# Performance work log

Hardware: AMD Instinct MI355X
Metric: run time of the kernel (lower is better)

## Reference

```python
import jax, jax.numpy as jnp
import numpy as np

N = 2048
D_IN = 128
D_OUT = 128
H = 8
EDGE_DIM = 8
EDGE_HID = 32
NEG_SLOPE = 0.2


def setup_inputs() -> dict:
    key = jax.random.key(0)
    ks = jax.random.split(key, 9)
    return {
        "inputs": jax.random.normal(ks[0], (N, D_IN), dtype=jnp.float32),
        "adj": jax.random.randint(ks[1], (N, N), 0, 2, dtype=jnp.int32),
        "edge_attr": jax.random.normal(ks[2], (N, N, EDGE_DIM), dtype=jnp.float32),
        # Linear weights stored as [in, out] (y = x @ W)
        "Wq": jax.random.normal(ks[3], (D_IN, D_OUT), dtype=jnp.float32) * 0.05,
        "Wk": jax.random.normal(ks[4], (D_IN, D_OUT), dtype=jnp.float32) * 0.05,
        "Wv": jax.random.normal(ks[5], (D_IN, D_OUT), dtype=jnp.float32) * 0.05,
        "We": jax.random.normal(ks[6], (EDGE_DIM, EDGE_HID), dtype=jnp.float32) * 0.05,
        "Wr": jax.random.normal(ks[7], (EDGE_HID, D_OUT), dtype=jnp.float32) * 0.05,
        "Wo": jax.random.normal(ks[8], (D_OUT, D_OUT), dtype=jnp.float32) * 0.05,
    }


def reference(inputs, adj, edge_attr, Wq, Wk, Wv, We, Wr, Wo):
    n = inputs.shape[0]
    dh = D_OUT // H  # head dim = 16
    # Projections -> [H, N, dh]
    Q = (inputs @ Wq).reshape(n, H, dh).transpose(1, 0, 2)
    K = (inputs @ Wk).reshape(n, H, dh).transpose(1, 0, 2)
    V = (inputs @ Wv).reshape(n, H, dh).transpose(1, 0, 2)
    # Edge bias: r_ij = W_r(W_e(e_ij)) viewed per-head; bias_hij = q_hi . r_ijh.
    # Fold We@Wr and contract with Q first to avoid materializing [N,N,D_OUT].
    Wer = (We @ Wr).reshape(EDGE_DIM, H, dh)          # [E, H, dh]
    QW = jnp.einsum('hid,ehd->hie', Q, Wer)           # [H, N, E]
    scores = (jnp.einsum('hid,hjd->hij', Q, K)
              + jnp.einsum('hie,ije->hij', QW, edge_attr)) / jnp.sqrt(jnp.float32(dh))
    scores = jax.nn.leaky_relu(scores, NEG_SLOPE)
    # Adjacency mask: only attend along existing edges
    scores = jnp.where((adj > 0)[None, :, :], scores, jnp.float32(-1e9))
    attn = jax.nn.softmax(scores, axis=-1)            # dropout is identity in eval
    out = jnp.einsum('hij,hjd->hid', attn, V)         # [H, N, dh]
    out = out.transpose(1, 0, 2).reshape(n, D_OUT)
    return out @ Wo
```

## Files before the change

kernel.cpp:

```cpp
#include <hip/hip_runtime.h>
#include <math.h>

#define NN 2048
#define DD 128
#define HH 8
#define DHH 16
#define EDIM 8
#define EHID 32

__global__ __launch_bounds__(384) void proj_kernel(
    const float* __restrict__ X,
    const float* __restrict__ Wq, const float* __restrict__ Wk,
    const float* __restrict__ Wv, const float* __restrict__ We,
    const float* __restrict__ Wr,
    float* __restrict__ Qo, float* __restrict__ Ko,
    float* __restrict__ Vo, float* __restrict__ QWo) {
  __shared__ float x_lds[2][128];
  __shared__ float wer_lds[8][128];
  __shared__ float q_lds[2][128];
  const int t = threadIdx.x;
  const int i0 = blockIdx.x * 2;

  if (t < 256) x_lds[t >> 7][t & 127] = X[(size_t)i0 * 128 + t];

  if (t < 128) {
    float acc[EDIM];
#pragma unroll
    for (int e = 0; e < EDIM; ++e) acc[e] = 0.f;
    for (int k = 0; k < EHID; ++k) {
      const float wr = Wr[k * 128 + t];
#pragma unroll
      for (int e = 0; e < EDIM; ++e) acc[e] = fmaf(We[e * EHID + k], wr, acc[e]);
    }
#pragma unroll
    for (int e = 0; e < EDIM; ++e) wer_lds[e][t] = acc[e];
  }
  __syncthreads();

  const int mat = t >> 7;
  const int c = t & 127;
  const float* __restrict__ W = (mat == 0) ? Wq : ((mat == 1) ? Wk : Wv);
  float a0 = 0.f, a1 = 0.f;
#pragma unroll 8
  for (int d = 0; d < 128; ++d) {
    const float w = W[d * 128 + c];
    a0 = fmaf(x_lds[0][d], w, a0);
    a1 = fmaf(x_lds[1][d], w, a1);
  }
  float* __restrict__ Out = (mat == 0) ? Qo : ((mat == 1) ? Ko : Vo);
  Out[(size_t)i0 * 128 + c] = a0;
  Out[(size_t)(i0 + 1) * 128 + c] = a1;
  if (mat == 0) { q_lds[0][c] = a0; q_lds[1][c] = a1; }
  __syncthreads();

  if (t < 64) {
    const int h = t >> 3, e = t & 7;
#pragma unroll
    for (int r = 0; r < 2; ++r) {
      float s = 0.f;
#pragma unroll
      for (int d = 0; d < DHH; ++d)
        s = fmaf(q_lds[r][h * DHH + d], wer_lds[e][h * DHH + d], s);
      QWo[(size_t)(i0 + r) * 64 + h * 8 + e] = s;
    }
  }
}

#define LOADEK(S, P) do {                                           \
    const int _j0 = (P) * 2;                                        \
    const float4* _e = ep + 2 * _j0;                                \
    e##S##0 = _e[0]; e##S##1 = _e[1]; e##S##2 = _e[2]; e##S##3 = _e[3]; \
    const float4* _k = kp + (size_t)_j0 * 32;                       \
    k##S##0 = _k[0];  k##S##1 = _k[1];  k##S##2 = _k[2];  k##S##3 = _k[3]; \
    k##S##4 = _k[32]; k##S##5 = _k[33]; k##S##6 = _k[34]; k##S##7 = _k[35]; \
  } while (0)

__global__ __launch_bounds__(512) void attn_kernel(
    const float* __restrict__ Qg, const float* __restrict__ Kg,
    const float* __restrict__ Vg, const float* __restrict__ QWg,
    const int* __restrict__ adj, const float* __restrict__ Eg,
    const float* __restrict__ Wo, float* __restrict__ out) {
  const int t = threadIdx.x;
  const int il = t & 3;
  const int h = (t >> 2) & 7;
  const int jo = t >> 5;
  const int i0 = blockIdx.x * 4;
  const int i = i0 + il;

  float4 q0, q1, q2, q3, qw0, qw1;
  {
    const float4* qp = (const float4*)(Qg + (size_t)i * 128 + h * 16);
    q0 = qp[0]; q1 = qp[1]; q2 = qp[2]; q3 = qp[3];
    const float4* wp = (const float4*)(QWg + (size_t)i * 64 + h * 8);
    qw0 = wp[0]; qw1 = wp[1];
  }

  float acc[16];
#pragma unroll
  for (int d = 0; d < 16; ++d) acc[d] = 0.f;
  float m = -INFINITY, mt = -INFINITY, l = 0.f;

  const int jbase = jo * 128;
  const int4* __restrict__ ap4 = (const int4*)(adj + (size_t)i * NN + jbase);
  const float4* __restrict__ ep = (const float4*)Eg + ((size_t)i * NN + jbase) * 2;
  const float4* __restrict__ kp = (const float4*)Kg + (size_t)jbase * 32 + h * 4;
  const float4* __restrict__ vp = (const float4*)Vg + (size_t)jbase * 32 + h * 4;

  auto score = [&](const float4 E0, const float4 E1,
                   const float4 K0, const float4 K1, const float4 K2, const float4 K3,
                   const int a) -> float {
    float s0 = q0.x * K0.x;    s0 = fmaf(q0.y, K0.y, s0);
    s0 = fmaf(q0.z, K0.z, s0); s0 = fmaf(q0.w, K0.w, s0);
    s0 = fmaf(q1.x, K1.x, s0); s0 = fmaf(q1.y, K1.y, s0);
    s0 = fmaf(q1.z, K1.z, s0); s0 = fmaf(q1.w, K1.w, s0);
    float s1 = q2.x * K2.x;    s1 = fmaf(q2.y, K2.y, s1);
    s1 = fmaf(q2.z, K2.z, s1); s1 = fmaf(q2.w, K2.w, s1);
    s1 = fmaf(q3.x, K3.x, s1); s1 = fmaf(q3.y, K3.y, s1);
    s1 = fmaf(q3.z, K3.z, s1); s1 = fmaf(q3.w, K3.w, s1);
    float b0 = qw0.x * E0.x;   b0 = fmaf(qw0.y, E0.y, b0);
    b0 = fmaf(qw0.z, E0.z, b0); b0 = fmaf(qw0.w, E0.w, b0);
    b0 = fmaf(qw1.x, E1.x, b0); b0 = fmaf(qw1.y, E1.y, b0);
    b0 = fmaf(qw1.z, E1.z, b0); b0 = fmaf(qw1.w, E1.w, b0);
    const float raw = (s0 + s1) + b0;
    float sc2 = fmaf(0.14426950f, fabsf(raw), 0.21640425f * raw);
    sc2 = (a > 0) ? sc2 : -1e9f;
    if (sc2 > mt) {
      const float r = exp2f(m - sc2);
      l *= r;
#pragma unroll
      for (int d = 0; d < 16; ++d) acc[d] *= r;
      m = sc2; mt = sc2 + 12.f;
    }
    const float p = exp2f(sc2 - m);
    l += p;
    return p;
  };
  auto pv = [&](const float p, const float4 V0, const float4 V1,
                const float4 V2, const float4 V3) {
    acc[0]  = fmaf(p, V0.x, acc[0]);  acc[1]  = fmaf(p, V0.y, acc[1]);
    acc[2]  = fmaf(p, V0.z, acc[2]);  acc[3]  = fmaf(p, V0.w, acc[3]);
    acc[4]  = fmaf(p, V1.x, acc[4]);  acc[5]  = fmaf(p, V1.y, acc[5]);
    acc[6]  = fmaf(p, V1.z, acc[6]);  acc[7]  = fmaf(p, V1.w, acc[7]);
    acc[8]  = fmaf(p, V2.x, acc[8]);  acc[9]  = fmaf(p, V2.y, acc[9]);
    acc[10] = fmaf(p, V2.z, acc[10]); acc[11] = fmaf(p, V2.w, acc[11]);
    acc[12] = fmaf(p, V3.x, acc[12]); acc[13] = fmaf(p, V3.y, acc[13]);
    acc[14] = fmaf(p, V3.z, acc[14]); acc[15] = fmaf(p, V3.w, acc[15]);
  };

  float4 eA0, eA1, eA2, eA3, kA0, kA1, kA2, kA3, kA4, kA5, kA6, kA7;
  float4 eB0, eB1, eB2, eB3, kB0, kB1, kB2, kB3, kB4, kB5, kB6, kB7;

  int4 a_cur = ap4[0];
  LOADEK(A, 0);
#pragma unroll 1
  for (int p2 = 0; p2 < 64; p2 += 2) {
    const int g = p2 >> 1;
    const int4 a_nxt = ap4[g < 31 ? g + 1 : 31];
    LOADEK(B, p2 + 1);
    {
      const float4* _v = vp + (size_t)(p2 * 2) * 32;
      const float4 v0 = _v[0],  v1 = _v[1],  v2 = _v[2],  v3 = _v[3];
      const float4 v4 = _v[32], v5 = _v[33], v6 = _v[34], v7 = _v[35];
      const float pa = score(eA0, eA1, kA0, kA1, kA2, kA3, a_cur.x);
      pv(pa, v0, v1, v2, v3);
      const float pb = score(eA2, eA3, kA4, kA5, kA6, kA7, a_cur.y);
      pv(pb, v4, v5, v6, v7);
    }
    LOADEK(A, p2 + 2 < 64 ? p2 + 2 : 63);
    {
      const float4* _v = vp + (size_t)(p2 * 2 + 2) * 32;
      const float4 v0 = _v[0],  v1 = _v[1],  v2 = _v[2],  v3 = _v[3];
      const float4 v4 = _v[32], v5 = _v[33], v6 = _v[34], v7 = _v[35];
      const float pa = score(eB0, eB1, kB0, kB1, kB2, kB3, a_cur.z);
      pv(pa, v0, v1, v2, v3);
      const float pb = score(eB2, eB3, kB4, kB5, kB6, kB7, a_cur.w);
      pv(pb, v4, v5, v6, v7);
    }
    a_cur = a_nxt;
  }

  __shared__ float mbuf[256 * 18];
  __shared__ float o_lds[4][128];
  const int u = t & 31;
  for (int k = 8; k >= 1; k >>= 1) {
    if (jo >= k && jo < 2 * k) {
      float* b = mbuf + ((size_t)((jo - k) * 32 + u)) * 18;
      b[0] = m; b[1] = l;
#pragma unroll
      for (int d = 0; d < 16; ++d) b[2 + d] = acc[d];
    }
    __syncthreads();
    if (jo < k) {
      const float* b = mbuf + ((size_t)(jo * 32 + u)) * 18;
      const float m2 = b[0], l2 = b[1];
      const float M = fmaxf(m, m2);
      const float sa = exp2f(m - M);
      const float sb = exp2f(m2 - M);
      l = l * sa + l2 * sb;
#pragma unroll
      for (int d = 0; d < 16; ++d) acc[d] = acc[d] * sa + b[2 + d] * sb;
      m = M;
    }
    __syncthreads();
  }

  if (jo == 0) {
    const float inv = 1.f / l;
#pragma unroll
    for (int d = 0; d < 16; ++d) o_lds[il][h * 16 + d] = acc[d] * inv;
  }
  __syncthreads();

  const int r = t >> 7;
  const int c = t & 127;
  float s = 0.f;
#pragma unroll 8
  for (int d = 0; d < 128; ++d)
    s = fmaf(o_lds[r][d], Wo[d * 128 + c], s);
  out[(size_t)(i0 + r) * 128 + c] = s;
}

extern "C" void kernel_launch(void* const* d_in, const int* in_sizes, int n_in,
                              void* d_out, int out_size, void* d_ws, size_t ws_size,
                              hipStream_t stream) {
  const float* X   = (const float*)d_in[0];
  const int*   adj = (const int*)d_in[1];
  const float* E   = (const float*)d_in[2];
  const float* Wq  = (const float*)d_in[3];
  const float* Wk  = (const float*)d_in[4];
  const float* Wv  = (const float*)d_in[5];
  const float* We  = (const float*)d_in[6];
  const float* Wr  = (const float*)d_in[7];
  const float* Wo  = (const float*)d_in[8];
  float* out = (float*)d_out;

  float* Qs  = (float*)d_ws;
  float* Ks  = Qs + (size_t)NN * DD;
  float* Vs  = Ks + (size_t)NN * DD;
  float* QWs = Vs + (size_t)NN * DD;

  hipLaunchKernelGGL(proj_kernel, dim3(NN / 2), dim3(384), 0, stream,
                     X, Wq, Wk, Wv, We, Wr, Qs, Ks, Vs, QWs);
  hipLaunchKernelGGL(attn_kernel, dim3(NN / 4), dim3(512), 0, stream,
                     Qs, Ks, Vs, QWs, adj, E, Wo, out);
}
```

Before: 442.3 us.

## Warp-specialize attention with async global-to-LDS producer and ring buffer

The attention kernel is split into a producer wave and consumer waves. The producer wave streams K, V and edge-attribute tiles into a 4-slot LDS ring with global_load_lds and vmcnt waits. The consumer waves read these tiles from LDS and run the online-softmax accumulation, with the two roles kept in step by matched s_barrier calls. Blocks now cover 2 query rows instead of 4. The aim is to overlap global loads with compute and share K/V through LDS instead of per-thread global loads. In exchange the kernel adds a barrier per key step, gets less K/V reuse per block, and relies on the barrier counts of both roles matching exactly.

```diff
diff --git a/kernel.cpp b/kernel.cpp
--- a/kernel.cpp
+++ b/kernel.cpp
@@ -7,6 +7,9 @@
 #define DHH 16
 #define EDIM 8
 #define EHID 32
+
+typedef __attribute__((address_space(1))) const void GV;
+typedef __attribute__((address_space(3))) void LV;
 
 __global__ __launch_bounds__(384) void proj_kernel(
     const float* __restrict__ X,
@@ -66,158 +69,194 @@
   }
 }
 
-#define LOADEK(S, P) do {                                           \
-    const int _j0 = (P) * 2;                                        \
-    const float4* _e = ep + 2 * _j0;                                \
-    e##S##0 = _e[0]; e##S##1 = _e[1]; e##S##2 = _e[2]; e##S##3 = _e[3]; \
-    const float4* _k = kp + (size_t)_j0 * 32;                       \
-    k##S##0 = _k[0];  k##S##1 = _k[1];  k##S##2 = _k[2];  k##S##3 = _k[3]; \
-    k##S##4 = _k[32]; k##S##5 = _k[33]; k##S##6 = _k[34]; k##S##7 = _k[35]; \
-  } while (0)
-
-__global__ __launch_bounds__(512) void attn_kernel(
+__global__ __launch_bounds__(320) void attn_kernel(
     const float* __restrict__ Qg, const float* __restrict__ Kg,
     const float* __restrict__ Vg, const float* __restrict__ QWg,
     const int* __restrict__ adj, const float* __restrict__ Eg,
     const float* __restrict__ Wo, float* __restrict__ out) {
+  __shared__ float4 Ks_lds[4][512];
+  __shared__ float4 Vs_lds[4][512];
+  __shared__ float4 Es_lds[4][64];
+  __shared__ float mbuf[128 * 18];
+  __shared__ float o_lds[2][128];
+
   const int t = threadIdx.x;
-  const int il = t & 3;
-  const int h = (t >> 2) & 7;
-  const int jo = t >> 5;
-  const int i0 = blockIdx.x * 4;
-  const int i = i0 + il;
-
-  float4 q0, q1, q2, q3, qw0, qw1;
-  {
-    const float4* qp = (const float4*)(Qg + (size_t)i * 128 + h * 16);
-    q0 = qp[0]; q1 = qp[1]; q2 = qp[2]; q3 = qp[3];
-    const float4* wp = (const float4*)(QWg + (size_t)i * 64 + h * 8);
-    qw0 = wp[0]; qw1 = wp[1];
-  }
-
-  float acc[16];
-#pragma unroll
-  for (int d = 0; d < 16; ++d) acc[d] = 0.f;
-  float m = -INFINITY, mt = -INFINITY, l = 0.f;
-
-  const int jbase = jo * 128;
-  const int4* __restrict__ ap4 = (const int4*)(adj + (size_t)i * NN + jbase);
-  const float4* __restrict__ ep = (const float4*)Eg + ((size_t)i * NN + jbase) * 2;
-  const float4* __restrict__ kp = (const float4*)Kg + (size_t)jbase * 32 + h * 4;
-  const float4* __restrict__ vp = (const float4*)Vg + (size_t)jbase * 32 + h * 4;
-
-  auto score = [&](const float4 E0, const float4 E1,
-                   const float4 K0, const float4 K1, const float4 K2, const float4 K3,
-                   const int a) -> float {
-    float s0 = q0.x * K0.x;    s0 = fmaf(q0.y, K0.y, s0);
-    s0 = fmaf(q0.z, K0.z, s0); s0 = fmaf(q0.w, K0.w, s0);
-    s0 = fmaf(q1.x, K1.x, s0); s0 = fmaf(q1.y, K1.y, s0);
-    s0 = fmaf(q1.z, K1.z, s0); s0 = fmaf(q1.w, K1.w, s0);
-    float s1 = q2.x * K2.x;    s1 = fmaf(q2.y, K2.y, s1);
-    s1 = fmaf(q2.z, K2.z, s1); s1 = fmaf(q2.w, K2.w, s1);
-    s1 = fmaf(q3.x, K3.x, s1); s1 = fmaf(q3.y, K3.y, s1);
-    s1 = fmaf(q3.z, K3.z, s1); s1 = fmaf(q3.w, K3.w, s1);
-    float b0 = qw0.x * E0.x;   b0 = fmaf(qw0.y, E0.y, b0);
-    b0 = fmaf(qw0.z, E0.z, b0); b0 = fmaf(qw0.w, E0.w, b0);
-    b0 = fmaf(qw1.x, E1.x, b0); b0 = fmaf(qw1.y, E1.y, b0);
-    b0 = fmaf(qw1.z, E1.z, b0); b0 = fmaf(qw1.w, E1.w, b0);
-    const float raw = (s0 + s1) + b0;
-    float sc2 = fmaf(0.14426950f, fabsf(raw), 0.21640425f * raw);
-    sc2 = (a > 0) ? sc2 : -1e9f;
-    if (sc2 > mt) {
-      const float r = exp2f(m - sc2);
-      l *= r;
-#pragma unroll
-      for (int d = 0; d < 16; ++d) acc[d] *= r;
-      m = sc2; mt = sc2 + 12.f;
-    }
-    const float p = exp2f(sc2 - m);
-    l += p;
-    return p;
-  };
-  auto pv = [&](const float p, const float4 V0, const float4 V1,
-                const float4 V2, const float4 V3) {
-    acc[0]  = fmaf(p, V0.x, acc[0]);  acc[1]  = fmaf(p, V0.y, acc[1]);
-    acc[2]  = fmaf(p, V0.z, acc[2]);  acc[3]  = fmaf(p, V0.w, acc[3]);
-    acc[4]  = fmaf(p, V1.x, acc[4]);  acc[5]  = fmaf(p, V1.y, acc[5]);
-    acc[6]  = fmaf(p, V1.z, acc[6]);  acc[7]  = fmaf(p, V1.w, acc[7]);
-    acc[8]  = fmaf(p, V2.x, acc[8]);  acc[9]  = fmaf(p, V2.y, acc[9]);
-    acc[10] = fmaf(p, V2.z, acc[10]); acc[11] = fmaf(p, V2.w, acc[11]);
-    acc[12] = fmaf(p, V3.x, acc[12]); acc[13] = fmaf(p, V3.y, acc[13]);
-    acc[14] = fmaf(p, V3.z, acc[14]); acc[15] = fmaf(p, V3.w, acc[15]);
-  };
-
-  float4 eA0, eA1, eA2, eA3, kA0, kA1, kA2, kA3, kA4, kA5, kA6, kA7;
-  float4 eB0, eB1, eB2, eB3, kB0, kB1, kB2, kB3, kB4, kB5, kB6, kB7;
-
-  int4 a_cur = ap4[0];
-  LOADEK(A, 0);
-#pragma unroll 1
-  for (int p2 = 0; p2 < 64; p2 += 2) {
-    const int g = p2 >> 1;
-    const int4 a_nxt = ap4[g < 31 ? g + 1 : 31];
-    LOADEK(B, p2 + 1);
+  const int i0 = blockIdx.x * 2;
+
+  if (t >= 256) {
+    const int lid = t - 256;
+    const int hi = lid >> 5;
+    const int r = lid & 31;
+    const int h_p = r & 7, qq_p = r >> 3;
+    const float* Kbase = Kg + (size_t)hi * 16384 + h_p * 16 + qq_p * 4;
+    const float* Vbase = Vg + (size_t)hi * 16384 + h_p * 16 + qq_p * 4;
+    const int il_e = lid >> 5;
+    const int jo_e = (lid & 31) >> 1, half = lid & 1;
+    const float* Ebase = Eg + ((size_t)(i0 + il_e) * 2048 + jo_e * 128) * 8 + half * 4;
+
+    auto ISSUE = [&](int slot, int jj) {
+      const float* kb = Kbase + (size_t)jj * 128;
+      const float* vb = Vbase + (size_t)jj * 128;
+      const float* eb = Ebase + (size_t)jj * 8;
+#pragma unroll
+      for (int j = 0; j < 8; ++j)
+        __builtin_amdgcn_global_load_lds((GV*)(kb + j * 32768),
+                                         (LV*)&Ks_lds[slot][j * 64], 16, 0, 0);
+#pragma unroll
+      for (int j = 0; j < 8; ++j)
+        __builtin_amdgcn_global_load_lds((GV*)(vb + j * 32768),
+                                         (LV*)&Vs_lds[slot][j * 64], 16, 0, 0);
+      __builtin_amdgcn_global_load_lds((GV*)eb, (LV*)&Es_lds[slot][0], 16, 0, 0);
+    };
+
+    ISSUE(0, 0); ISSUE(1, 1); ISSUE(2, 2);
+    asm volatile("s_waitcnt vmcnt(34)" ::: "memory");
+    __builtin_amdgcn_s_barrier();
+    __builtin_amdgcn_sched_barrier(0);
+    for (int jj = 0; jj < 128; ++jj) {
+      if (jj < 125) {
+        ISSUE((jj + 3) & 3, jj + 3);
+        asm volatile("s_waitcnt vmcnt(34)" ::: "memory");
+      } else if (jj == 125) {
+        asm volatile("s_waitcnt vmcnt(17)" ::: "memory");
+      } else {
+        asm volatile("s_waitcnt vmcnt(0)" ::: "memory");
+      }
+      __builtin_amdgcn_s_barrier();
+      __builtin_amdgcn_sched_barrier(0);
+    }
+  } else {
+    const int il = t & 1;
+    const int h = (t >> 1) & 7;
+    const int jo = t >> 4;
+    const int i = i0 + il;
+
+    float4 q0, q1, q2, q3, qw0, qw1;
     {
-      const float4* _v = vp + (size_t)(p2 * 2) * 32;
-      const float4 v0 = _v[0],  v1 = _v[1],  v2 = _v[2],  v3 = _v[3];
-      const float4 v4 = _v[32], v5 = _v[33], v6 = _v[34], v7 = _v[35];
-      const float pa = score(eA0, eA1, kA0, kA1, kA2, kA3, a_cur.x);
-      pv(pa, v0, v1, v2, v3);
-      const float pb = score(eA2, eA3, kA4, kA5, kA6, kA7, a_cur.y);
-      pv(pb, v4, v5, v6, v7);
-    }
-    LOADEK(A, p2 + 2 < 64 ? p2 + 2 : 63);
+      const float4* qp = (const float4*)(Qg + (size_t)i * 128 + h * 16);
+      q0 = qp[0]; q1 = qp[1]; q2 = qp[2]; q3 = qp[3];
+      const float4* wp = (const float4*)(QWg + (size_t)i * 64 + h * 8);
+      qw0 = wp[0]; qw1 = wp[1];
+    }
+
+    float acc[16];
+#pragma unroll
+    for (int d = 0; d < 16; ++d) acc[d] = 0.f;
+    float m = -INFINITY, mt = -INFINITY, l = 0.f;
+
+    const int4* __restrict__ ap4 = (const int4*)(adj + (size_t)i * NN + jo * 128);
+
+    auto score = [&](const float4 E0, const float4 E1,
+                     const float4 K0, const float4 K1, const float4 K2,
+                     const float4 K3, const int a) -> float {
+      float s0 = q0.x * K0.x;    s0 = fmaf(q0.y, K0.y, s0);
+      s0 = fmaf(q0.z, K0.z, s0); s0 = fmaf(q0.w, K0.w, s0);
+      s0 = fmaf(q1.x, K1.x, s0); s0 = fmaf(q1.y, K1.y, s0);
+      s0 = fmaf(q1.z, K1.z, s0); s0 = fmaf(q1.w, K1.w, s0);
+      float s1 = q2.x * K2.x;    s1 = fmaf(q2.y, K2.y, s1);
+      s1 = fmaf(q2.z, K2.z, s1); s1 = fmaf(q2.w, K2.w, s1);
+      s1 = fmaf(q3.x, K3.x, s1); s1 = fmaf(q3.y, K3.y, s1);
+      s1 = fmaf(q3.z, K3.z, s1); s1 = fmaf(q3.w, K3.w, s1);
+      float b0 = qw0.x * E0.x;    b0 = fmaf(qw0.y, E0.y, b0);
+      b0 = fmaf(qw0.z, E0.z, b0); b0 = fmaf(qw0.w, E0.w, b0);
+      b0 = fmaf(qw1.x, E1.x, b0); b0 = fmaf(qw1.y, E1.y, b0);
+      b0 = fmaf(qw1.z, E1.z, b0); b0 = fmaf(qw1.w, E1.w, b0);
+      const float raw = (s0 + s1) + b0;
+      float sc2 = fmaf(0.14426950f, fabsf(raw), 0.21640425f * raw);
+      sc2 = (a > 0) ? sc2 : -1e9f;
+      if (sc2 > mt) {
+        const float rr = exp2f(m - sc2);
+        l *= rr;
+#pragma unroll
+        for (int d = 0; d < 16; ++d) acc[d] *= rr;
+        m = sc2; mt = sc2 + 12.f;
+      }
+      const float p = exp2f(sc2 - m);
+      l += p;
+      return p;
+    };
+    auto pv = [&](const float p, const float4 V0, const float4 V1,
+                  const float4 V2, const float4 V3) {
+      acc[0]  = fmaf(p, V0.x, acc[0]);  acc[1]  = fmaf(p, V0.y, acc[1]);
+      acc[2]  = fmaf(p, V0.z, acc[2]);  acc[3]  = fmaf(p, V0.w, acc[3]);
+      acc[4]  = fmaf(p, V1.x, acc[4]);  acc[5]  = fmaf(p, V1.y, acc[5]);
+      acc[6]  = fmaf(p, V1.z, acc[6]);  acc[7]  = fmaf(p, V1.w, acc[7]);
+      acc[8]  = fmaf(p, V2.x, acc[8]);  acc[9]  = fmaf(p, V2.y, acc[9]);
+      acc[10] = fmaf(p, V2.z, acc[10]); acc[11] = fmaf(p, V2.w, acc[11]);
+      acc[12] = fmaf(p, V3.x, acc[12]); acc[13] = fmaf(p, V3.y, acc[13]);
+      acc[14] = fmaf(p, V3.z, acc[14]); acc[15] = fmaf(p, V3.w, acc[15]);
+    };
+
+    int4 a_cur = ap4[0];
+    __builtin_amdgcn_s_barrier();
+    __builtin_amdgcn_sched_barrier(0);
+
+    for (int j4 = 0; j4 < 32; ++j4) {
+      const int4 a_nxt = ap4[j4 < 31 ? j4 + 1 : 31];
+#pragma unroll
+      for (int u4 = 0; u4 < 4; ++u4) {
+        const int jj = j4 * 4 + u4;
+        const int slot = jj & 3;
+        const int a = (u4 == 0) ? a_cur.x : (u4 == 1) ? a_cur.y
+                    : (u4 == 2) ? a_cur.z : a_cur.w;
+        const float4* kq = &Ks_lds[slot][jo * 32 + h];
+        const float4 K0 = kq[0], K1 = kq[8], K2 = kq[16], K3 = kq[24];
+        const float4* vq = &Vs_lds[slot][jo * 32 + h];
+        const float4 V0 = vq[0], V1 = vq[8], V2 = vq[16], V3 = vq[24];
+        const float4* eq = &Es_lds[slot][il * 32 + jo * 2];
+        const float4 E0 = eq[0], E1 = eq[1];
+        const float p = score(E0, E1, K0, K1, K2, K3, a);
+        pv(p, V0, V1, V2, V3);
+        __builtin_amdgcn_s_barrier();
+        __builtin_amdgcn_sched_barrier(0);
+      }
+      a_cur = a_nxt;
+    }
+
     {
-      const float4* _v = vp + (size_t)(p2 * 2 + 2) * 32;
-      const float4 v0 = _v[0],  v1 = _v[1],  v2 = _v[2],  v3 = _v[3];
-      const float4 v4 = _v[32], v5 = _v[33], v6 = _v[34], v7 = _v[35];
-      const float pa = score(eB0, eB1, kB0, kB1, kB2, kB3, a_cur.z);
-      pv(pa, v0, v1, v2, v3);
-      const float pb = score(eB2, eB3, kB4, kB5, kB6, kB7, a_cur.w);
-      pv(pb, v4, v5, v6, v7);
-    }
-    a_cur = a_nxt;
-  }
-
-  __shared__ float mbuf[256 * 18];
-  __shared__ float o_lds[4][128];
-  const int u = t & 31;
-  for (int k = 8; k >= 1; k >>= 1) {
-    if (jo >= k && jo < 2 * k) {
-      float* b = mbuf + ((size_t)((jo - k) * 32 + u)) * 18;
-      b[0] = m; b[1] = l;
-#pragma unroll
-      for (int d = 0; d < 16; ++d) b[2 + d] = acc[d];
+      const int u = t & 15;
+      (void)u;
     }
     __syncthreads();
-    if (jo < k) {
-      const float* b = mbuf + ((size_t)(jo * 32 + u)) * 18;
-      const float m2 = b[0], l2 = b[1];
-      const float M = fmaxf(m, m2);
-      const float sa = exp2f(m - M);
-      const float sb = exp2f(m2 - M);
-      l = l * sa + l2 * sb;
-#pragma unroll
-      for (int d = 0; d < 16; ++d) acc[d] = acc[d] * sa + b[2 + d] * sb;
-      m = M;
+    const int u = t & 15;
+    for (int k = 8; k >= 1; k >>= 1) {
+      if (jo >= k && jo < 2 * k) {
+        float* b = mbuf + ((size_t)((jo - k) * 16 + u)) * 18;
+        b[0] = m; b[1] = l;
+#pragma unroll
+        for (int d = 0; d < 16; ++d) b[2 + d] = acc[d];
+      }
+      __syncthreads();
+      if (jo < k) {
+        const float* b = mbuf + ((size_t)(jo * 16 + u)) * 18;
+        const float m2 = b[0], l2 = b[1];
+        const float M = fmaxf(m, m2);
+        const float sa = exp2f(m - M), sb = exp2f(m2 - M);
+        l = l * sa + l2 * sb;
+#pragma unroll
+        for (int d = 0; d < 16; ++d) acc[d] = acc[d] * sa + b[2 + d] * sb;
+        m = M;
+      }
+      __syncthreads();
+    }
+    if (jo == 0) {
+      const float inv = 1.f / l;
+#pragma unroll
+      for (int d = 0; d < 16; ++d) o_lds[il][h * 16 + d] = acc[d] * inv;
     }
     __syncthreads();
-  }
-
-  if (jo == 0) {
-    const float inv = 1.f / l;
-#pragma unroll
-    for (int d = 0; d < 16; ++d) o_lds[il][h * 16 + d] = acc[d] * inv;
-  }
-  __syncthreads();
-
-  const int r = t >> 7;
-  const int c = t & 127;
-  float s = 0.f;
+    const int r = t >> 7, c = t & 127;
+    float s = 0.f;
 #pragma unroll 8
-  for (int d = 0; d < 128; ++d)
-    s = fmaf(o_lds[r][d], Wo[d * 128 + c], s);
-  out[(size_t)(i0 + r) * 128 + c] = s;
+    for (int d = 0; d < 128; ++d)
+      s = fmaf(o_lds[r][d], Wo[d * 128 + c], s);
+    out[(size_t)(i0 + r) * 128 + c] = s;
+    return;
+  }
+
+  __syncthreads();
+  for (int k = 8; k >= 1; k >>= 1) { __syncthreads(); __syncthreads(); }
+  __syncthreads();
 }
 
 extern "C" void kernel_launch(void* const* d_in, const int* in_sizes, int n_in,
@@ -241,6 +280,6 @@
 
   hipLaunchKernelGGL(proj_kernel, dim3(NN / 2), dim3(384), 0, stream,
                      X, Wq, Wk, Wv, We, Wr, Qs, Ks, Vs, QWs);
-  hipLaunchKernelGGL(attn_kernel, dim3(NN / 4), dim3(512), 0, stream,
+  hipLaunchKernelGGL(attn_kernel, dim3(NN / 2), dim3(320), 0, stream,
                      Qs, Ks, Vs, QWs, adj, E, Wo, out);
 }
```

After: 360.7 us. 18.4% less time.
